# Kernel tuning notes

Hardware: AMD Instinct MI355X
Metric: run time of the kernel (lower is better)

## Reference

```python
import jax, jax.numpy as jnp
import numpy as np

L, H, M, KB = 8, 512, 32, 256  # layers, hidden, fourier modes, key bits
EPS = 1e-5


def setup_inputs() -> dict:
    key = jax.random.key(0)
    ks = jax.random.split(key, 20)
    B, S = 8, 2048
    s = 0.02
    return {
        'x': jax.random.normal(ks[0], (B, S), jnp.float32),
        # input projection Linear(1, H): weight [H] (squeezed), bias [H]
        'in_w': jax.random.normal(ks[1], (H,), jnp.float32) * s,
        'in_b': jax.random.normal(ks[2], (H,), jnp.float32) * s,
        # per-layer fourier weights (complex, stored as real/imag), conv1d(k=1), layernorm
        'fw_r': jax.random.normal(ks[3], (L, M, H, H), jnp.float32) * s,
        'fw_i': jax.random.normal(ks[4], (L, M, H, H), jnp.float32) * s,
        'conv_w': jax.random.normal(ks[5], (L, H, H), jnp.float32) / np.sqrt(H),
        'conv_b': jax.random.normal(ks[6], (L, H), jnp.float32) * s,
        'ln_g': jnp.ones((L, H), jnp.float32),
        'ln_b': jnp.zeros((L, H), jnp.float32),
        # output projection H -> H/2 -> H/4 -> 1
        'op1_w': jax.random.normal(ks[7], (H // 2, H), jnp.float32) / np.sqrt(H),
        'op1_b': jnp.zeros((H // 2,), jnp.float32),
        'op2_w': jax.random.normal(ks[8], (H // 4, H // 2), jnp.float32) / np.sqrt(H // 2),
        'op2_b': jnp.zeros((H // 4,), jnp.float32),
        'op3_w': jax.random.normal(ks[9], (1, H // 4), jnp.float32) / np.sqrt(H // 4),
        'op3_b': jnp.zeros((1,), jnp.float32),
        # cryptanalytic head H -> H -> KB (sigmoid)
        'h1_w': jax.random.normal(ks[10], (H, H), jnp.float32) / np.sqrt(H),
        'h1_b': jnp.zeros((H,), jnp.float32),
        'h2_w': jax.random.normal(ks[11], (KB, H), jnp.float32) / np.sqrt(H),
        'h2_b': jnp.zeros((KB,), jnp.float32),
    }


def _gelu(x):
    return jax.nn.gelu(x, approximate=False)


def _fourier_layer(x, Wc, cw, cb, g, b):
    # x: [B, S, H]; Wc: [M, H, H] complex
    S = x.shape[1]
    x_ft = jnp.fft.rfft(x, axis=1)  # [B, F, H] complex, F = S//2+1
    m = min(M, x_ft.shape[1])
    # batched per-mode complex GEMM (replaces python loop over modes)
    spec = jnp.einsum('bmh,mhk->bmk', x_ft[:, :m], Wc[:m])
    out_ft = jnp.concatenate([spec, jnp.zeros_like(x_ft[:, m:])], axis=1)
    x_fourier = jnp.fft.irfft(out_ft, n=S, axis=1)  # real [B, S, H]
    x_conv = x @ cw.T + cb  # Conv1d kernel-size-1 == per-position linear
    y = x_fourier + x_conv
    mu = jnp.mean(y, axis=-1, keepdims=True)
    var = jnp.var(y, axis=-1, keepdims=True)
    return (y - mu) * jax.lax.rsqrt(var + EPS) * g + b


def reference(x, in_w, in_b, fw_r, fw_i, conv_w, conv_b, ln_g, ln_b,
              op1_w, op1_b, op2_w, op2_b, op3_w, op3_b,
              h1_w, h1_b, h2_w, h2_b):
    # input projection: Linear(1, H) on x[..., None]
    h = x[:, :, None] * in_w[None, None, :] + in_b  # [B, S, H]
    Wc = fw_r + 1j * fw_i  # [L, M, H, H]
    for l in range(L):
        h = _fourier_layer(h, Wc[l], conv_w[l], conv_b[l], ln_g[l], ln_b[l]) + h
    # output projection (dropout is identity in eval)
    o = _gelu(h @ op1_w.T + op1_b)
    o = _gelu(o @ op2_w.T + op2_b)
    output = (o @ op3_w.T + op3_b)[..., 0]  # [B, S]
    gf = jnp.mean(h, axis=1)  # [B, H]
    k = _gelu(gf @ h1_w.T + h1_b)
    key_pred = jax.nn.sigmoid(k @ h2_w.T + h2_b)  # [B, KB]
    return output, key_pred
```

## Files before the change

kernel.cpp:

```cpp
#include <hip/hip_runtime.h>
#include <hip/hip_bf16.h>
#include <math.h>

#define BB   8
#define SEQ  2048
#define HD   512
#define LAY  8
#define MD   32
#define NKB  256
#define LNEPS 1e-5f

typedef __attribute__((ext_vector_type(8))) short v8s;
typedef __attribute__((ext_vector_type(4))) float v4f;
typedef __attribute__((ext_vector_type(4))) unsigned short v4us;

__device__ __forceinline__ float b2f(__hip_bfloat16 v) { return __bfloat162float(v); }
__device__ __forceinline__ float geluf(float v) { return v * 0.5f * (1.f + erff(v * 0.70710678118654752f)); }
__device__ __forceinline__ float bflo(unsigned int u) { return __uint_as_float((u & 0xFFFFu) << 16); }
__device__ __forceinline__ float bfhi(unsigned int u) { return __uint_as_float(u & 0xFFFF0000u); }

__device__ __forceinline__ float ldin(const void* p, size_t i, int bf) {
    if (bf) return __bfloat162float(((const __hip_bfloat16*)p)[i]);
    return ((const float*)p)[i];
}
__device__ __forceinline__ void stout(void* p, size_t i, float v, int bf) {
    if (bf) ((__hip_bfloat16*)p)[i] = __float2bfloat16(v);
    else    ((float*)p)[i] = v;
}

__device__ __forceinline__ void gl2lds16(const void* g, void* l) {
    __builtin_amdgcn_global_load_lds((__attribute__((address_space(1))) void*)g,
                                     (__attribute__((address_space(3))) void*)l, 16, 0, 0);
}

__global__ void k_flag(const unsigned int* __restrict__ lng_bits, int* __restrict__ flag) {
    if (threadIdx.x == 0 && blockIdx.x == 0)
        *flag = (lng_bits[0] == 0x3F803F80u) ? 1 : 0;
}

__global__ void k_setup(const void* __restrict__ x, const void* __restrict__ in_w, const void* __restrict__ in_b,
                        const void* __restrict__ cw, const void* __restrict__ w1, const void* __restrict__ w2,
                        const void* __restrict__ h1w, const void* __restrict__ h2w,
                        __hip_bfloat16* __restrict__ Ffwd, __hip_bfloat16* __restrict__ T2,
                        __hip_bfloat16* __restrict__ cwbf, __hip_bfloat16* __restrict__ w1bf,
                        __hip_bfloat16* __restrict__ w2bf, float* __restrict__ h1T, float* __restrict__ h2T,
                        float* __restrict__ h, __hip_bfloat16* __restrict__ hbf,
                        float* __restrict__ gf,
                        const int* __restrict__ flag) {
    int bf = *flag;
    int blk = blockIdx.x, t = threadIdx.x;
    if (blk < 512) {
        int idx = blk * 256 + t;
        int j = idx >> 11, s = idx & 2047;
        int m = j >> 1;
        int phase = (m * s) & (SEQ - 1);
        float ang = (float)phase * (6.283185307179586f / (float)SEQ);
        Ffwd[idx] = __float2bfloat16((j & 1) ? -sinf(ang) : cosf(ang));
    } else if (blk < 1024) {
        int idx = (blk - 512) * 256 + t;
        int s = idx >> 6, j = idx & 63;
        int m = j >> 1;
        float v;
        if (j == 0)      v = 1.f / (float)SEQ;
        else if (j == 1) v = 0.f;
        else {
            int phase = (m * s) & (SEQ - 1);
            float ang = (float)phase * (6.283185307179586f / (float)SEQ);
            v = (j & 1) ? (-2.f / (float)SEQ) * sinf(ang) : (2.f / (float)SEQ) * cosf(ang);
        }
        T2[idx] = __float2bfloat16(v);
    } else if (blk < 9216) {
        int idx = (blk - 1024) * 256 + t;
        cwbf[idx] = __float2bfloat16(ldin(cw, idx, bf));
    } else if (blk < 9728) {
        int idx = (blk - 9216) * 256 + t;
        w1bf[idx] = __float2bfloat16(ldin(w1, idx, bf));
    } else if (blk < 9856) {
        int idx = (blk - 9728) * 256 + t;
        w2bf[idx] = __float2bfloat16(ldin(w2, idx, bf));
    } else if (blk < 10880) {
        int idx = (blk - 9856) * 256 + t;
        int r = idx & 511, c = idx >> 9;
        h1T[idx] = ldin(h1w, (size_t)r * 512 + c, bf);
    } else if (blk < 11392) {
        int idx = (blk - 10880) * 256 + t;
        int r = idx & 255, c = idx >> 8;
        h2T[idx] = ldin(h2w, (size_t)r * 512 + c, bf);
    } else if (blk < 11408) {
        int idx = (blk - 11392) * 256 + t;
        gf[idx] = 0.f;
    } else {
        int idx = (blk - 11408) * 256 + t;
        int j = idx & 511;
        int bs = idx >> 9;
        float v = ldin(x, bs, bf) * ldin(in_w, j, bf) + ldin(in_b, j, bf);
        h[idx] = v;
        hbf[idx] = __float2bfloat16(v);
    }
}

__global__ __launch_bounds__(256) void k_fdft2(const __hip_bfloat16* __restrict__ hbf,
                                               const __hip_bfloat16* __restrict__ Ffwd,
                                               float* __restrict__ Xpart) {
    __shared__ __align__(16) __hip_bfloat16 Als[2][16 * 72];
    int t = threadIdx.x;
    int lane = t & 63, wv = t >> 6;
    int ln15 = lane & 15, quad = lane >> 4;
    int ht = blockIdx.x, b = blockIdx.y, kh = blockIdx.z;
    int kcs = kh * 16;
    int sr = t >> 2, hc = (t & 3) * 4;

    v4f acc = (v4f){0.f, 0.f, 0.f, 0.f};

    const __hip_bfloat16* asrc0 = hbf + (size_t)b * SEQ * HD + ht * 16;
    const __hip_bfloat16* fbase = Ffwd + (size_t)(wv * 16 + ln15) * SEQ + quad * 8;

    v4us cur = *(const v4us*)(asrc0 + (size_t)(kcs * 64 + sr) * HD + hc);
#pragma unroll
    for (int e = 0; e < 4; e++)
        Als[0][(hc + e) * 72 + sr] = ((const __hip_bfloat16*)&cur)[e];
    __syncthreads();
    for (int i = 0; i < 16; i++) {
        int buf = i & 1;
        v4us nxt = cur;
        if (i < 15)
            nxt = *(const v4us*)(asrc0 + (size_t)((kcs + i + 1) * 64 + sr) * HD + hc);
        v8s bf0 = *(const v8s*)(fbase + (kcs + i) * 64);
        v8s bf1 = *(const v8s*)(fbase + (kcs + i) * 64 + 32);
        v8s af0 = *(const v8s*)&Als[buf][ln15 * 72 + quad * 8];
        v8s af1 = *(const v8s*)&Als[buf][ln15 * 72 + 32 + quad * 8];
        acc = __builtin_amdgcn_mfma_f32_16x16x32_bf16(af0, bf0, acc, 0, 0, 0);
        acc = __builtin_amdgcn_mfma_f32_16x16x32_bf16(af1, bf1, acc, 0, 0, 0);
        if (i < 15) {
#pragma unroll
            for (int e = 0; e < 4; e++)
                Als[buf ^ 1][(hc + e) * 72 + sr] = ((const __hip_bfloat16*)&nxt)[e];
        }
        __syncthreads();
        cur = nxt;
    }
    int j = wv * 16 + ln15;
    int m = j >> 1, c = j & 1;
    int hg = ht * 16 + quad * 4;
    float* outp = Xpart + (size_t)kh * 262144 + (size_t)(b * 32 + m) * 1024;
#pragma unroll
    for (int r = 0; r < 4; r++)
        outp[(size_t)(hg + r) * 2 + c] = acc[r];
}

__global__ __launch_bounds__(512) void k_mix(const float* __restrict__ Xp0, const float* __restrict__ Xp1,
                                             const void* __restrict__ fwr, const void* __restrict__ fwi,
                                             __hip_bfloat16* __restrict__ spec2, int l,
                                             const int* __restrict__ flag) {
    int bf = *flag;
    int kt = blockIdx.x;
    int m  = blockIdx.y;
    int t = threadIdx.x;
    int kl = t & 15, hg = t >> 4;
    int k0 = kt * 64 + kl * 4;
    __shared__ float xs[8192];
    __shared__ float red[32 * 512];
    for (int e = t; e < 8192; e += 512) {
        int bb = e >> 10, r = e & 1023;
        size_t off = (size_t)(bb * 32 + m) * 1024 + r;
        xs[bb * 1024 + r] = Xp0[off] + Xp1[off];
    }
    __syncthreads();
    float ar[8][4], ai[8][4];
#pragma unroll
    for (int bb = 0; bb < 8; bb++)
#pragma unroll
        for (int q = 0; q < 4; q++) { ar[bb][q] = 0.f; ai[bb][q] = 0.f; }
    size_t wbase = (size_t)(l * 32 + m) * 262144 + k0;
    const float2* xs2 = (const float2*)xs;
    if (bf) {
        const __hip_bfloat16* fr = (const __hip_bfloat16*)fwr;
        const __hip_bfloat16* fi = (const __hip_bfloat16*)fwi;
#pragma unroll 2
        for (int hh = hg; hh < 512; hh += 32) {
            v4us urv = *(const v4us*)(fr + wbase + (size_t)hh * 512);
            v4us uiv = *(const v4us*)(fi + wbase + (size_t)hh * 512);
            float wr[4], wi[4];
#pragma unroll
            for (int q = 0; q < 4; q++) {
                wr[q] = __uint_as_float(((unsigned int)(unsigned short)urv[q]) << 16);
                wi[q] = __uint_as_float(((unsigned int)(unsigned short)uiv[q]) << 16);
            }
#pragma unroll
            for (int bb = 0; bb < 8; bb++) {
                float2 x2 = xs2[bb * 512 + hh];
#pragma unroll
                for (int q = 0; q < 4; q++) {
                    ar[bb][q] += x2.x * wr[q] - x2.y * wi[q];
                    ai[bb][q] += x2.x * wi[q] + x2.y * wr[q];
                }
            }
        }
    } else {
        const float* fr = (const float*)fwr;
        const float* fi = (const float*)fwi;
#pragma unroll 2
        for (int hh = hg; hh < 512; hh += 32) {
            v4f wrv = *(const v4f*)(fr + wbase + (size_t)hh * 512);
            v4f wiv = *(const v4f*)(fi + wbase + (size_t)hh * 512);
#pragma unroll
            for (int bb = 0; bb < 8; bb++) {
                float2 x2 = xs2[bb * 512 + hh];
#pragma unroll
                for (int q = 0; q < 4; q++) {
                    ar[bb][q] += x2.x * wrv[q] - x2.y * wiv[q];
                    ai[bb][q] += x2.x * wiv[q] + x2.y * wrv[q];
                }
            }
        }
    }
    v4f* red4 = (v4f*)red;
#pragma unroll
    for (int bb = 0; bb < 8; bb++)
        red4[hg * 128 + bb * 16 + kl] = (v4f){ar[bb][0], ar[bb][1], ar[bb][2], ar[bb][3]};
    __syncthreads();
    float sr = 0.f;
#pragma unroll
    for (int g = 0; g < 32; g++) sr += red[g * 512 + t];
    __syncthreads();
#pragma unroll
    for (int bb = 0; bb < 8; bb++)
        red4[hg * 128 + bb * 16 + kl] = (v4f){ai[bb][0], ai[bb][1], ai[bb][2], ai[bb][3]};
    __syncthreads();
    float si = 0.f;
#pragma unroll
    for (int g = 0; g < 32; g++) si += red[g * 512 + t];

    int bb = t >> 6, j = t & 63;
    int k = kt * 64 + j;
    size_t o = ((size_t)(bb * 512 + k) << 6) + 2 * m;
    __hip_bfloat16 hr = __float2bfloat16(sr), hi = __float2bfloat16(si);
    unsigned int pk = (unsigned int)*(unsigned short*)&hr | ((unsigned int)*(unsigned short*)&hi << 16);
    *(unsigned int*)(spec2 + o) = pk;
}

__global__ __launch_bounds__(512) void k_gln(__hip_bfloat16* __restrict__ hbf,
                                             const __hip_bfloat16* __restrict__ cwbf,
                                             const __hip_bfloat16* __restrict__ T2,
                                             const __hip_bfloat16* __restrict__ spec2,
                                             const void* __restrict__ cb,
                                             const void* __restrict__ lng, const void* __restrict__ lnb,
                                             float* __restrict__ h,
                                             int l, const int* __restrict__ flag) {
    int bfv = *flag;
    __shared__ __align__(16) __hip_bfloat16 smem[2][18432];
    __shared__ float stats[128];
    __hip_bfloat16* Yls = &smem[0][0];

    int t = threadIdx.x;
    int lane = t & 63, wv = t >> 6;
    int wr = wv >> 2, wc = wv & 3;
    int ln15 = lane & 15, quad = lane >> 4;
    int row0 = blockIdx.x * 64;
    int b = row0 >> 11, s0 = row0 & 2047;

    v4f acc[16];
#pragma unroll
    for (int i = 0; i < 16; i++) acc[i] = (v4f){0.f, 0.f, 0.f, 0.f};

    const __hip_bfloat16* cwl = cwbf + (size_t)l * 262144;

    auto stage = [&](int buf, int kc) {
        int k0 = kc * 32;
        if (t < 256) {
            int row = t >> 2, kq = (t & 3) * 8;
            const __hip_bfloat16* asrc = (k0 < 512)
                ? hbf + (size_t)(row0 + row) * 512 + k0 + kq
                : T2 + (size_t)(s0 + row) * 64 + (k0 - 512) + kq;
            gl2lds16(asrc, &smem[buf][(size_t)(wv * 64) * 8]);
        }
#pragma unroll
        for (int p = 0; p < 4; p++) {
            int i = p * 512 + t;
            int n = i >> 2, kq = (i & 3) * 8;
            const __hip_bfloat16* bsrc = (k0 < 512)
                ? cwl + (size_t)n * 512 + k0 + kq
                : spec2 + (size_t)(b * 512 + n) * 64 + (k0 - 512) + kq;
            gl2lds16(bsrc, &smem[buf][2048 + (size_t)(p * 512 + wv * 64) * 8]);
        }
    };

    stage(0, 0);
    __syncthreads();
    int cur = 0;
    for (int kc = 0; kc < 18; kc++) {
        if (kc < 17) stage(cur ^ 1, kc + 1);
        const __hip_bfloat16* Als = &smem[cur][0];
        const __hip_bfloat16* Bls = &smem[cur][2048];
        v8s af[2], bfr[8];
#pragma unroll
        for (int i = 0; i < 2; i++)
            af[i] = *(const v8s*)&Als[(wr * 32 + i * 16 + ln15) * 32 + quad * 8];
#pragma unroll
        for (int j = 0; j < 8; j++)
            bfr[j] = *(const v8s*)&Bls[(wc * 128 + j * 16 + ln15) * 32 + quad * 8];
#pragma unroll
        for (int i = 0; i < 2; i++)
#pragma unroll
            for (int j = 0; j < 8; j++)
                acc[i * 8 + j] = __builtin_amdgcn_mfma_f32_16x16x32_bf16(af[i], bfr[j], acc[i * 8 + j], 0, 0, 0);
        __syncthreads();
        cur ^= 1;
    }
#pragma unroll
    for (int j = 0; j < 8; j++) {
        int col = wc * 128 + j * 16 + ln15;
        float cbv = ldin(cb, l * HD + col, bfv);
#pragma unroll
        for (int i = 0; i < 2; i++) {
            int rl = wr * 32 + i * 16 + quad * 4;
#pragma unroll
            for (int r = 0; r < 4; r++)
                Yls[(rl + r) * 520 + col] = __float2bfloat16(acc[i * 8 + j][r] + cbv);
        }
    }
    __syncthreads();
    {
        int r = t >> 3, g = t & 7;
        float s = 0.f, q = 0.f;
        for (int i = 0; i < 32; i++) {
            int cp = g + i * 8;
            unsigned int u = *(const unsigned int*)&Yls[r * 520 + cp * 2];
            float v0 = bflo(u), v1 = bfhi(u);
            s += v0 + v1; q += v0 * v0 + v1 * v1;
        }
        s += __shfl_xor(s, 1); s += __shfl_xor(s, 2); s += __shfl_xor(s, 4);
        q += __shfl_xor(q, 1); q += __shfl_xor(q, 2); q += __shfl_xor(q, 4);
        if (g == 0) {
            float mu = s * (1.f / (float)HD);
            float var = q * (1.f / (float)HD) - mu * mu;
            stats[r * 2] = mu; stats[r * 2 + 1] = rsqrtf(var + LNEPS);
        }
    }
    __syncthreads();
    {
        int c2 = t & 255;
        int gc = 2 * c2;
        float g0 = ldin(lng, l * HD + gc, bfv),     g1 = ldin(lng, l * HD + gc + 1, bfv);
        float b0 = ldin(lnb, l * HD + gc, bfv),     b1 = ldin(lnb, l * HD + gc + 1, bfv);
        int rbase = t >> 8;
        for (int k = 0; k < 32; k++) {
            int r = rbase + 2 * k;
            float mu = stats[r * 2], rs = stats[r * 2 + 1];
            unsigned int u = *(const unsigned int*)&Yls[r * 520 + c2 * 2];
            float v0 = bflo(u), v1 = bfhi(u);
            float2 hv = *(const float2*)&h[(size_t)(row0 + r) * HD + gc];
            float n0 = (v0 - mu) * rs * g0 + b0 + hv.x;
            float n1 = (v1 - mu) * rs * g1 + b1 + hv.y;
            *(float2*)&h[(size_t)(row0 + r) * HD + gc] = (float2){n0, n1};
            __hip_bfloat16 a0 = __float2bfloat16(n0), a1 = __float2bfloat16(n1);
            unsigned int up = ((unsigned int)(*(unsigned short*)&a1) << 16) | (unsigned int)(*(unsigned short*)&a0);
            ((unsigned int*)(hbf + (size_t)(row0 + r) * HD))[c2] = up;
        }
    }
}

__global__ __launch_bounds__(256) void k_pj1(const __hip_bfloat16* __restrict__ hbf,
                                             const __hip_bfloat16* __restrict__ w1bf,
                                             const void* __restrict__ b1,
                                             __hip_bfloat16* __restrict__ o1bf,
                                             const int* __restrict__ flag) {
    int bfv = *flag;
    __shared__ __align__(16) __hip_bfloat16 smem[2][8192];
    int t = threadIdx.x;
    int lane = t & 63, wv = t >> 6;
    int wr = wv >> 1, wc = wv & 1;
    int ln15 = lane & 15, quad = lane >> 4;
    int row0 = blockIdx.x * 128, n0 = blockIdx.y * 128;

    v4f acc[16];
#pragma unroll
    for (int i = 0; i < 16; i++) acc[i] = (v4f){0.f, 0.f, 0.f, 0.f};

    auto stage = [&](int buf, int kc) {
        int k0 = kc * 32;
#pragma unroll
        for (int p = 0; p < 2; p++) {
            int i = p * 256 + t;
            int row = i >> 2, kq = (i & 3) * 8;
            gl2lds16(hbf + (size_t)(row0 + row) * 512 + k0 + kq, &smem[buf][(size_t)(p * 256 + wv * 64) * 8]);
            gl2lds16(w1bf + (size_t)(n0 + row) * 512 + k0 + kq, &smem[buf][4096 + (size_t)(p * 256 + wv * 64) * 8]);
        }
    };

    stage(0, 0);
    __syncthreads();
    int cur = 0;
    for (int kc = 0; kc < 16; kc++) {
        if (kc < 15) stage(cur ^ 1, kc + 1);
        const __hip_bfloat16* Als = &smem[cur][0];
        const __hip_bfloat16* Bls = &smem[cur][4096];
        v8s af[4], bfr[4];
#pragma unroll
        for (int i = 0; i < 4; i++)
            af[i] = *(const v8s*)&Als[(wr * 64 + i * 16 + ln15) * 32 + quad * 8];
#pragma unroll
        for (int j = 0; j < 4; j++)
            bfr[j] = *(const v8s*)&Bls[(wc * 64 + j * 16 + ln15) * 32 + quad * 8];
#pragma unroll
        for (int i = 0; i < 4; i++)
#pragma unroll
            for (int j = 0; j < 4; j++)
                acc[i * 4 + j] = __builtin_amdgcn_mfma_f32_16x16x32_bf16(af[i], bfr[j], acc[i * 4 + j], 0, 0, 0);
        __syncthreads();
        cur ^= 1;
    }
#pragma unroll
    for (int j = 0; j < 4; j++) {
        int col = n0 + wc * 64 + j * 16 + ln15;
        float bv = ldin(b1, col, bfv);
#pragma unroll
        for (int i = 0; i < 4; i++) {
            int rg = row0 + wr * 64 + i * 16 + quad * 4;
#pragma unroll
            for (int r = 0; r < 4; r++)
                o1bf[(size_t)(rg + r) * 256 + col] = __float2bfloat16(geluf(acc[i * 4 + j][r] + bv));
        }
    }
}

__global__ __launch_bounds__(256) void k_pj2(const __hip_bfloat16* __restrict__ o1bf,
                                             const __hip_bfloat16* __restrict__ w2bf,
                                             const void* __restrict__ b2,
                                             const void* __restrict__ w3, const void* __restrict__ b3,
                                             void* __restrict__ out, const int* __restrict__ flag) {
    int bfv = *flag;
    __shared__ __align__(16) __hip_bfloat16 smem[2][8192];
    __shared__ __hip_bfloat16 o2s[128 * 130];
    __shared__ float w3s[128];
    int t = threadIdx.x;
    int lane = t & 63, wv = t >> 6;
    int wr = wv >> 1, wc = wv & 1;
    int ln15 = lane & 15, quad = lane >> 4;
    int row0 = blockIdx.x * 128;
    if (t < 128) w3s[t] = ldin(w3, t, bfv);

    v4f acc[16];
#pragma unroll
    for (int i = 0; i < 16; i++) acc[i] = (v4f){0.f, 0.f, 0.f, 0.f};

    auto stage = [&](int buf, int kc) {
        int k0 = kc * 32;
#pragma unroll
        for (int p = 0; p < 2; p++) {
            int i = p * 256 + t;
            int row = i >> 2, kq = (i & 3) * 8;
            gl2lds16(o1bf + (size_t)(row0 + row) * 256 + k0 + kq, &smem[buf][(size_t)(p * 256 + wv * 64) * 8]);
            gl2lds16(w2bf + (size_t)row * 256 + k0 + kq,          &smem[buf][4096 + (size_t)(p * 256 + wv * 64) * 8]);
        }
    };

    stage(0, 0);
    __syncthreads();
    int cur = 0;
    for (int kc = 0; kc < 8; kc++) {
        if (kc < 7) stage(cur ^ 1, kc + 1);
        const __hip_bfloat16* Als = &smem[cur][0];
        const __hip_bfloat16* Bls = &smem[cur][4096];
        v8s af[4], bfr[4];
#pragma unroll
        for (int i = 0; i < 4; i++)
            af[i] = *(const v8s*)&Als[(wr * 64 + i * 16 + ln15) * 32 + quad * 8];
#pragma unroll
        for (int j = 0; j < 4; j++)
            bfr[j] = *(const v8s*)&Bls[(wc * 64 + j * 16 + ln15) * 32 + quad * 8];
#pragma unroll
        for (int i = 0; i < 4; i++)
#pragma unroll
            for (int j = 0; j < 4; j++)
                acc[i * 4 + j] = __builtin_amdgcn_mfma_f32_16x16x32_bf16(af[i], bfr[j], acc[i * 4 + j], 0, 0, 0);
        __syncthreads();
        cur ^= 1;
    }
#pragma unroll
    for (int j = 0; j < 4; j++) {
        int col = wc * 64 + j * 16 + ln15;
        float bv = ldin(b2, col, bfv);
#pragma unroll
        for (int i = 0; i < 4; i++) {
            int rl = wr * 64 + i * 16 + quad * 4;
#pragma unroll
            for (int r = 0; r < 4; r++)
                o2s[(rl + r) * 130 + col] = __float2bfloat16(geluf(acc[i * 4 + j][r] + bv));
        }
    }
    __syncthreads();
    if (t < 128) {
        float s = 0.f;
        for (int j = 0; j < 128; j++) s += b2f(o2s[t * 130 + j]) * w3s[j];
        stout(out, row0 + t, s + ldin(b3, 0, bfv), bfv);
    }
}

__global__ __launch_bounds__(512) void k_gf(const float* __restrict__ h, float* __restrict__ gf) {
    int sc = blockIdx.x, b = blockIdx.y;
    int j = threadIdx.x;
    const float* p = h + ((size_t)b * SEQ + sc * 64) * HD + j;
    float s = 0.f;
    for (int i = 0; i < 64; i++) s += p[(size_t)i * HD];
    atomicAdd(&gf[b * HD + j], s * (1.f / (float)SEQ));
}

__global__ __launch_bounds__(512) void k_head(const float* __restrict__ gf,
                                              const float* __restrict__ h1T, const void* __restrict__ h1b,
                                              const float* __restrict__ h2T, const void* __restrict__ h2b,
                                              void* __restrict__ out, const int* __restrict__ flag) {
    int bf = *flag;
    int b = blockIdx.x;
    int t = threadIdx.x;
    __shared__ float gs[512];
    __shared__ float ks[512];
    gs[t] = gf[b * HD + t];
    __syncthreads();
    float a = 0.f;
    for (int j = 0; j < 512; j++) a += gs[j] * h1T[j * 512 + t];
    ks[t] = geluf(a + ldin(h1b, t, bf));
    __syncthreads();
    if (t < 256) {
        float s = 0.f;
        for (int j = 0; j < 512; j++) s += ks[j] * h2T[j * 256 + t];
        s += ldin(h2b, t, bf);
        stout(out, BB * SEQ + b * NKB + t, 1.f / (1.f + expf(-s)), bf);
    }
}

extern "C" void kernel_launch(void* const* d_in, const int* in_sizes, int n_in,
                              void* d_out, int out_size, void* d_ws, size_t ws_size,
                              hipStream_t stream) {
    const void* x    = d_in[0];
    const void* in_w = d_in[1];
    const void* in_b = d_in[2];
    const void* fwr  = d_in[3];
    const void* fwi  = d_in[4];
    const void* cw   = d_in[5];
    const void* cb   = d_in[6];
    const void* lng  = d_in[7];
    const void* lnb  = d_in[8];
    const void* w1   = d_in[9];
    const void* b1   = d_in[10];
    const void* w2   = d_in[11];
    const void* b2   = d_in[12];
    const void* w3   = d_in[13];
    const void* b3   = d_in[14];
    const void* h1w  = d_in[15];
    const void* h1b  = d_in[16];
    const void* h2w  = d_in[17];
    const void* h2b  = d_in[18];

    float* ws = (float*)d_ws;
    __hip_bfloat16* Ffwd = (__hip_bfloat16*)ws;
    float*          h    = ws + 131072;
    float*          Xp   = h + 8388608;
    __hip_bfloat16* o1bf = (__hip_bfloat16*)Xp;
    __hip_bfloat16* hbf  = (__hip_bfloat16*)(Xp + 4194304);
    __hip_bfloat16* cwbf = (__hip_bfloat16*)(Xp + 8388608);
    __hip_bfloat16* T2   = (__hip_bfloat16*)(Xp + 10485760);
    __hip_bfloat16* spec2= (__hip_bfloat16*)(Xp + 10551296);
    float*          XftOld = Xp + 10682368;
    float*          gf   = XftOld + 262144;
    float*          w1T  = gf + 4096;
    __hip_bfloat16* w1bf = (__hip_bfloat16*)w1T;
    __hip_bfloat16* w2bf = (__hip_bfloat16*)(w1T + 65536);
    float*          w2T  = w1T + 131072;
    float*          h1T  = w2T + 32768;
    float*          h2T  = h1T + 262144;
    int*            flag = (int*)(h2T + 131072);
    float*          Xpart = h2T + 131072 + 64;

    k_flag<<<1, 1, 0, stream>>>((const unsigned int*)lng, flag);
    k_setup<<<44176, 256, 0, stream>>>(x, in_w, in_b, cw, w1, w2, h1w, h2w,
                                       Ffwd, T2, cwbf, w1bf, w2bf, h1T, h2T,
                                       h, hbf, gf, flag);

    for (int l = 0; l < LAY; l++) {
        k_fdft2<<<dim3(32, 8, 2), 256, 0, stream>>>(hbf, Ffwd, Xpart);
        k_mix<<<dim3(8, 32), 512, 0, stream>>>(Xpart, Xpart + 262144, fwr, fwi, spec2, l, flag);
        k_gln<<<256, 512, 0, stream>>>(hbf, cwbf, T2, spec2, cb, lng, lnb, h, l, flag);
    }

    k_gf<<<dim3(32, 8), 512, 0, stream>>>(h, gf);
    k_pj1<<<dim3(128, 2), 256, 0, stream>>>(hbf, w1bf, b1, o1bf, flag);
    k_pj2<<<128, 256, 0, stream>>>(o1bf, w2bf, b2, w3, b3, d_out, flag);
    k_head<<<8, 512, 0, stream>>>(gf, h1T, h1b, h2T, h2b, d_out, flag);
}
```

Before: 1.189 ms.

## Drop per-layer bf16 copy of h; convert fp32 h to bf16 while staging tiles

Stops writing a bf16 shadow copy of the hidden state every layer (now only on the last layer, for the output projection). The forward-DFT and conv/LN GEMM kernels instead read fp32 h directly and convert to bf16 as they stage it into LDS. In the GEMM kernel this replaces the async global-to-LDS copy for the A tile with register loads and converts, using a padded LDS layout. This removes one bf16 store stream per layer but doubles the bytes read for the A operand, and loses the async LDS load path for A.

```diff
diff --git a/kernel.cpp b/kernel.cpp
--- a/kernel.cpp
+++ b/kernel.cpp
@@ -33,6 +33,11 @@
                                      (__attribute__((address_space(3))) void*)l, 16, 0, 0);
 }
 
+__device__ __forceinline__ unsigned short f2bfu(float f) {
+    __hip_bfloat16 b = __float2bfloat16(f);
+    return *(unsigned short*)&b;
+}
+
 __global__ void k_flag(const unsigned int* __restrict__ lng_bits, int* __restrict__ flag) {
     if (threadIdx.x == 0 && blockIdx.x == 0)
         *flag = (lng_bits[0] == 0x3F803F80u) ? 1 : 0;
@@ -44,7 +49,7 @@
                         __hip_bfloat16* __restrict__ Ffwd, __hip_bfloat16* __restrict__ T2,
                         __hip_bfloat16* __restrict__ cwbf, __hip_bfloat16* __restrict__ w1bf,
                         __hip_bfloat16* __restrict__ w2bf, float* __restrict__ h1T, float* __restrict__ h2T,
-                        float* __restrict__ h, __hip_bfloat16* __restrict__ hbf,
+                        float* __restrict__ h,
                         float* __restrict__ gf,
                         const int* __restrict__ flag) {
     int bf = *flag;
@@ -95,11 +100,10 @@
         int bs = idx >> 9;
         float v = ldin(x, bs, bf) * ldin(in_w, j, bf) + ldin(in_b, j, bf);
         h[idx] = v;
-        hbf[idx] = __float2bfloat16(v);
-    }
-}
-
-__global__ __launch_bounds__(256) void k_fdft2(const __hip_bfloat16* __restrict__ hbf,
+    }
+}
+
+__global__ __launch_bounds__(256) void k_fdft2(const float* __restrict__ h,
                                                const __hip_bfloat16* __restrict__ Ffwd,
                                                float* __restrict__ Xpart) {
     __shared__ __align__(16) __hip_bfloat16 Als[2][16 * 72];
@@ -112,19 +116,22 @@
 
     v4f acc = (v4f){0.f, 0.f, 0.f, 0.f};
 
-    const __hip_bfloat16* asrc0 = hbf + (size_t)b * SEQ * HD + ht * 16;
+    const float* asrc0 = h + (size_t)b * SEQ * HD + ht * 16;
     const __hip_bfloat16* fbase = Ffwd + (size_t)(wv * 16 + ln15) * SEQ + quad * 8;
 
-    v4us cur = *(const v4us*)(asrc0 + (size_t)(kcs * 64 + sr) * HD + hc);
-#pragma unroll
-    for (int e = 0; e < 4; e++)
-        Als[0][(hc + e) * 72 + sr] = ((const __hip_bfloat16*)&cur)[e];
+    float4 cur = *(const float4*)(asrc0 + (size_t)(kcs * 64 + sr) * HD + hc);
+    {
+        const float* cf = (const float*)&cur;
+#pragma unroll
+        for (int e = 0; e < 4; e++)
+            Als[0][(hc + e) * 72 + sr] = __float2bfloat16(cf[e]);
+    }
     __syncthreads();
     for (int i = 0; i < 16; i++) {
         int buf = i & 1;
-        v4us nxt = cur;
+        float4 nxt = cur;
         if (i < 15)
-            nxt = *(const v4us*)(asrc0 + (size_t)((kcs + i + 1) * 64 + sr) * HD + hc);
+            nxt = *(const float4*)(asrc0 + (size_t)((kcs + i + 1) * 64 + sr) * HD + hc);
         v8s bf0 = *(const v8s*)(fbase + (kcs + i) * 64);
         v8s bf1 = *(const v8s*)(fbase + (kcs + i) * 64 + 32);
         v8s af0 = *(const v8s*)&Als[buf][ln15 * 72 + quad * 8];
@@ -132,9 +139,10 @@
         acc = __builtin_amdgcn_mfma_f32_16x16x32_bf16(af0, bf0, acc, 0, 0, 0);
         acc = __builtin_amdgcn_mfma_f32_16x16x32_bf16(af1, bf1, acc, 0, 0, 0);
         if (i < 15) {
+            const float* nf = (const float*)&nxt;
 #pragma unroll
             for (int e = 0; e < 4; e++)
-                Als[buf ^ 1][(hc + e) * 72 + sr] = ((const __hip_bfloat16*)&nxt)[e];
+                Als[buf ^ 1][(hc + e) * 72 + sr] = __float2bfloat16(nf[e]);
         }
         __syncthreads();
         cur = nxt;
@@ -248,7 +256,7 @@
                                              float* __restrict__ h,
                                              int l, const int* __restrict__ flag) {
     int bfv = *flag;
-    __shared__ __align__(16) __hip_bfloat16 smem[2][18432];
+    __shared__ __align__(16) __hip_bfloat16 smem[2][19456];
     __shared__ float stats[128];
     __hip_bfloat16* Yls = &smem[0][0];
 
@@ -258,6 +266,7 @@
     int ln15 = lane & 15, quad = lane >> 4;
     int row0 = blockIdx.x * 64;
     int b = row0 >> 11, s0 = row0 & 2047;
+    int arow = t >> 3, acolq = (t & 7) * 4;
 
     v4f acc[16];
 #pragma unroll
@@ -265,15 +274,8 @@
 
     const __hip_bfloat16* cwl = cwbf + (size_t)l * 262144;
 
-    auto stage = [&](int buf, int kc) {
+    auto stageB = [&](int buf, int kc) {
         int k0 = kc * 32;
-        if (t < 256) {
-            int row = t >> 2, kq = (t & 3) * 8;
-            const __hip_bfloat16* asrc = (k0 < 512)
-                ? hbf + (size_t)(row0 + row) * 512 + k0 + kq
-                : T2 + (size_t)(s0 + row) * 64 + (k0 - 512) + kq;
-            gl2lds16(asrc, &smem[buf][(size_t)(wv * 64) * 8]);
-        }
 #pragma unroll
         for (int p = 0; p < 4; p++) {
             int i = p * 512 + t;
@@ -281,21 +283,50 @@
             const __hip_bfloat16* bsrc = (k0 < 512)
                 ? cwl + (size_t)n * 512 + k0 + kq
                 : spec2 + (size_t)(b * 512 + n) * 64 + (k0 - 512) + kq;
-            gl2lds16(bsrc, &smem[buf][2048 + (size_t)(p * 512 + wv * 64) * 8]);
+            gl2lds16(bsrc, &smem[buf][2560 + (size_t)(p * 512 + wv * 64) * 8]);
         }
     };
-
-    stage(0, 0);
+    auto loadA = [&](int kc, float4& av, v4us& tv) {
+        int k0 = kc * 32;
+        if (k0 < 512) {
+            av = *(const float4*)&h[(size_t)(row0 + arow) * HD + k0 + acolq];
+        } else {
+            tv = *(const v4us*)&T2[(size_t)(s0 + arow) * 64 + (k0 - 512) + acolq];
+        }
+    };
+    auto writeA = [&](int buf, int kc, const float4& av, const v4us& tv) {
+        __hip_bfloat16* dst = &smem[buf][arow * 40 + acolq];
+        if (kc * 32 < 512) {
+            const float* af = (const float*)&av;
+            v4us pk;
+#pragma unroll
+            for (int e = 0; e < 4; e++) pk[e] = (short)f2bfu(af[e]);
+            *(v4us*)dst = pk;
+        } else {
+            *(v4us*)dst = tv;
+        }
+    };
+
+    {
+        float4 av; v4us tv;
+        loadA(0, av, tv);
+        stageB(0, 0);
+        writeA(0, 0, av, tv);
+    }
     __syncthreads();
     int cur = 0;
+    float4 avn; v4us tvn;
     for (int kc = 0; kc < 18; kc++) {
-        if (kc < 17) stage(cur ^ 1, kc + 1);
+        if (kc < 17) {
+            loadA(kc + 1, avn, tvn);
+            stageB(cur ^ 1, kc + 1);
+        }
         const __hip_bfloat16* Als = &smem[cur][0];
-        const __hip_bfloat16* Bls = &smem[cur][2048];
+        const __hip_bfloat16* Bls = &smem[cur][2560];
         v8s af[2], bfr[8];
 #pragma unroll
         for (int i = 0; i < 2; i++)
-            af[i] = *(const v8s*)&Als[(wr * 32 + i * 16 + ln15) * 32 + quad * 8];
+            af[i] = *(const v8s*)&Als[(wr * 32 + i * 16 + ln15) * 40 + quad * 8];
 #pragma unroll
         for (int j = 0; j < 8; j++)
             bfr[j] = *(const v8s*)&Bls[(wc * 128 + j * 16 + ln15) * 32 + quad * 8];
@@ -304,6 +335,7 @@
 #pragma unroll
             for (int j = 0; j < 8; j++)
                 acc[i * 8 + j] = __builtin_amdgcn_mfma_f32_16x16x32_bf16(af[i], bfr[j], acc[i * 8 + j], 0, 0, 0);
+        if (kc < 17) writeA(cur ^ 1, kc + 1, avn, tvn);
         __syncthreads();
         cur ^= 1;
     }
@@ -321,17 +353,17 @@
     }
     __syncthreads();
     {
-        int r = t >> 3, g = t & 7;
+        int r = t >> 3, g2 = t & 7;
         float s = 0.f, q = 0.f;
         for (int i = 0; i < 32; i++) {
-            int cp = g + i * 8;
+            int cp = g2 + i * 8;
             unsigned int u = *(const unsigned int*)&Yls[r * 520 + cp * 2];
             float v0 = bflo(u), v1 = bfhi(u);
             s += v0 + v1; q += v0 * v0 + v1 * v1;
         }
         s += __shfl_xor(s, 1); s += __shfl_xor(s, 2); s += __shfl_xor(s, 4);
         q += __shfl_xor(q, 1); q += __shfl_xor(q, 2); q += __shfl_xor(q, 4);
-        if (g == 0) {
+        if (g2 == 0) {
             float mu = s * (1.f / (float)HD);
             float var = q * (1.f / (float)HD) - mu * mu;
             stats[r * 2] = mu; stats[r * 2 + 1] = rsqrtf(var + LNEPS);
@@ -344,6 +376,7 @@
         float g0 = ldin(lng, l * HD + gc, bfv),     g1 = ldin(lng, l * HD + gc + 1, bfv);
         float b0 = ldin(lnb, l * HD + gc, bfv),     b1 = ldin(lnb, l * HD + gc + 1, bfv);
         int rbase = t >> 8;
+        int last = (l == LAY - 1);
         for (int k = 0; k < 32; k++) {
             int r = rbase + 2 * k;
             float mu = stats[r * 2], rs = stats[r * 2 + 1];
@@ -353,9 +386,10 @@
             float n0 = (v0 - mu) * rs * g0 + b0 + hv.x;
             float n1 = (v1 - mu) * rs * g1 + b1 + hv.y;
             *(float2*)&h[(size_t)(row0 + r) * HD + gc] = (float2){n0, n1};
-            __hip_bfloat16 a0 = __float2bfloat16(n0), a1 = __float2bfloat16(n1);
-            unsigned int up = ((unsigned int)(*(unsigned short*)&a1) << 16) | (unsigned int)(*(unsigned short*)&a0);
-            ((unsigned int*)(hbf + (size_t)(row0 + r) * HD))[c2] = up;
+            if (last) {
+                unsigned int up = ((unsigned int)f2bfu(n1) << 16) | (unsigned int)f2bfu(n0);
+                ((unsigned int*)(hbf + (size_t)(row0 + r) * HD))[c2] = up;
+            }
         }
     }
 }
@@ -575,10 +609,10 @@
     k_flag<<<1, 1, 0, stream>>>((const unsigned int*)lng, flag);
     k_setup<<<44176, 256, 0, stream>>>(x, in_w, in_b, cw, w1, w2, h1w, h2w,
                                        Ffwd, T2, cwbf, w1bf, w2bf, h1T, h2T,
-                                       h, hbf, gf, flag);
+                                       h, gf, flag);
 
     for (int l = 0; l < LAY; l++) {
-        k_fdft2<<<dim3(32, 8, 2), 256, 0, stream>>>(hbf, Ffwd, Xpart);
+        k_fdft2<<<dim3(32, 8, 2), 256, 0, stream>>>(h, Ffwd, Xpart);
         k_mix<<<dim3(8, 32), 512, 0, stream>>>(Xpart, Xpart + 262144, fwr, fwi, spec2, l, flag);
         k_gln<<<256, 512, 0, stream>>>(hbf, cwbf, T2, spec2, cb, lng, lnb, h, l, flag);
     }
```

Result: no change. 1.167 ms (-1.9%).
